# Optimization experiments

Hardware: AMD Instinct MI355X
Metric: run time of the kernel (lower is better)

## Reference

```python
import jax, jax.numpy as jnp
from jax import lax
import numpy as np

B, T, H, K = 32, 512, 2048, 128


def setup_inputs() -> dict:
    key = jax.random.key(0)
    k1, k2, k3, k4, k5, k6, k7 = jax.random.split(key, 7)
    hiddens = jax.random.normal(k1, (B, T, H), dtype=jnp.float32)
    mask = jnp.ones((B, T), dtype=jnp.int32)  # mask[:,0] must be on (torchcrf)
    labels = jax.random.randint(k2, (B, T), 0, K)
    W = jax.random.normal(k3, (H, K), dtype=jnp.float32) * 0.02
    b = jnp.zeros((K,), dtype=jnp.float32)
    # torchcrf inits transitions uniform(-0.1, 0.1)
    start_transitions = jax.random.uniform(k4, (K,), minval=-0.1, maxval=0.1)
    end_transitions = jax.random.uniform(k5, (K,), minval=-0.1, maxval=0.1)
    transitions = jax.random.uniform(k6, (K, K), minval=-0.1, maxval=0.1)
    return {"hiddens": hiddens, "mask": mask, "labels": labels, "W": W, "b": b,
            "start_transitions": start_transitions, "end_transitions": end_transitions,
            "transitions": transitions}


def _crf_log_likelihood(emissions, tags, mask, start_t, end_t, trans):
    # emissions: [B,T,K], tags/mask: [B,T]
    Bn, Tn, Kn = emissions.shape
    maskf = mask.astype(emissions.dtype)
    # ---- numerator: score of the gold path ----
    score = start_t[tags[:, 0]] + emissions[jnp.arange(Bn), 0, tags[:, 0]]
    prev, cur = tags[:, :-1], tags[:, 1:]
    emit_cur = jnp.take_along_axis(emissions[:, 1:], cur[..., None], axis=-1)[..., 0]
    score = score + jnp.sum((trans[prev, cur] + emit_cur) * maskf[:, 1:], axis=1)
    last_idx = mask.sum(axis=1).astype(jnp.int32) - 1
    last_tags = jnp.take_along_axis(tags, last_idx[:, None], axis=1)[:, 0]
    score = score + end_t[last_tags]
    # ---- denominator: log partition via stable logsumexp scan ----
    def step(alpha, inp):
        emit_t, m_t = inp  # [B,K], [B]
        nxt = jax.nn.logsumexp(alpha[:, :, None] + trans[None] + emit_t[:, None, :], axis=1)
        alpha = jnp.where(m_t[:, None] > 0, nxt, alpha)
        return alpha, None
    alpha0 = start_t[None, :] + emissions[:, 0]
    emits = jnp.swapaxes(emissions[:, 1:], 0, 1)  # [T-1,B,K]
    ms = jnp.swapaxes(mask[:, 1:], 0, 1)          # [T-1,B]
    alpha, _ = lax.scan(step, alpha0, (emits, ms))
    logZ = jax.nn.logsumexp(alpha + end_t[None, :], axis=1)
    return score - logZ


def _viterbi_decode(emissions, mask, start_t, end_t, trans):
    Bn, Tn, Kn = emissions.shape
    tag_ids = jnp.arange(Kn, dtype=jnp.int32)
    def step(score, inp):
        emit_t, m_t = inp
        cand = score[:, :, None] + trans[None]          # [B,K,K] prev->cur
        bp = jnp.argmax(cand, axis=1).astype(jnp.int32)  # [B,K]
        best = jnp.max(cand, axis=1) + emit_t
        on = m_t[:, None] > 0
        new_score = jnp.where(on, best, score)
        bp = jnp.where(on, bp, tag_ids[None, :])  # identity for padded steps
        return new_score, bp
    score0 = start_t[None, :] + emissions[:, 0]
    emits = jnp.swapaxes(emissions[:, 1:], 0, 1)
    ms = jnp.swapaxes(mask[:, 1:], 0, 1)
    score, history = lax.scan(step, score0, (emits, ms))  # history: [T-1,B,K]
    last_tag = jnp.argmax(score + end_t[None, :], axis=1).astype(jnp.int32)  # [B]
    def back(tag, bp_t):
        tag = jnp.take_along_axis(bp_t, tag[:, None], axis=1)[:, 0]
        return tag, tag
    _, tags_prev = lax.scan(back, last_tag, history, reverse=True)  # [T-1,B]
    tags = jnp.concatenate([tags_prev, last_tag[None, :]], axis=0)  # [T,B]
    return jnp.swapaxes(tags, 0, 1)  # [B,T]


def reference(hiddens, mask, labels, W, b, start_transitions, end_transitions, transitions):
    logits = jnp.einsum('bth,hk->btk', hiddens, W) + b  # emission projection
    decode = _viterbi_decode(logits, mask, start_transitions, end_transitions, transitions)
    llh = _crf_log_likelihood(logits, labels, mask, start_transitions, end_transitions, transitions)
    loss = -jnp.mean(llh)  # -1 * crf(..., reduction='mean')
    return (decode, loss)
```

## Files before the change

kernel.cpp:

```cpp
#include <hip/hip_runtime.h>
#include <hip/hip_bf16.h>
#include <math.h>

#define BB 32
#define TT 512
#define HH 2048
#define KK 128

__global__ __launch_bounds__(512) void gemm_k(const float* __restrict__ hid,
                                              const float* __restrict__ Wm,
                                              const float* __restrict__ bias,
                                              float* __restrict__ logits,
                                              float* __restrict__ loss_slot) {
    __shared__ union {
        struct { float As[4][16][72]; float Bs[4][16][132]; } s;
        float4 red[16][128];
    } sm;
    const int tid = threadIdx.x, bid = blockIdx.x;
    if (bid == 0 && tid == 0) loss_slot[0] = 0.0f;
    const int g = tid >> 7, lt = tid & 127;
    const int rowBase = bid * 64;
    const int rowg = lt >> 4, colg = lt & 15;
    const int arow = lt >> 1, ahq = lt & 1;

    float acc[8][8];
#pragma unroll
    for (int i = 0; i < 8; i++)
#pragma unroll
        for (int j = 0; j < 8; j++) acc[i][j] = 0.0f;

    const float* hA = hid + (size_t)(rowBase + arow) * HH + g * 512 + ahq * 8;

    for (int it = 0; it < 32; ++it) {
        const int h0 = g * 512 + it * 16;
        float4 a0 = *(const float4*)(hA + it * 16);
        float4 a1 = *(const float4*)(hA + it * 16 + 4);
        float4 bv[4];
#pragma unroll
        for (int r = 0; r < 4; ++r) {
            int idx = r * 128 + lt;
            bv[r] = *(const float4*)(Wm + (size_t)(h0 + (idx >> 5)) * KK + (idx & 31) * 4);
        }
        __syncthreads();
        const int hb = ahq * 8;
        sm.s.As[g][hb + 0][arow] = a0.x;
        sm.s.As[g][hb + 1][arow] = a0.y;
        sm.s.As[g][hb + 2][arow] = a0.z;
        sm.s.As[g][hb + 3][arow] = a0.w;
        sm.s.As[g][hb + 4][arow] = a1.x;
        sm.s.As[g][hb + 5][arow] = a1.y;
        sm.s.As[g][hb + 6][arow] = a1.z;
        sm.s.As[g][hb + 7][arow] = a1.w;
#pragma unroll
        for (int r = 0; r < 4; ++r) {
            int idx = r * 128 + lt;
            *(float4*)&sm.s.Bs[g][idx >> 5][(idx & 31) * 4] = bv[r];
        }
        __syncthreads();
#pragma unroll
        for (int h = 0; h < 16; ++h) {
            float4 aL = *(const float4*)&sm.s.As[g][h][rowg * 8];
            float4 aH = *(const float4*)&sm.s.As[g][h][rowg * 8 + 4];
            float4 b0 = *(const float4*)&sm.s.Bs[g][h][colg * 4];
            float4 b1 = *(const float4*)&sm.s.Bs[g][h][64 + colg * 4];
            float ar[8] = {aL.x, aL.y, aL.z, aL.w, aH.x, aH.y, aH.z, aH.w};
            float br[8] = {b0.x, b0.y, b0.z, b0.w, b1.x, b1.y, b1.z, b1.w};
#pragma unroll
            for (int i = 0; i < 8; i++)
#pragma unroll
                for (int j = 0; j < 8; j++) acc[i][j] = fmaf(ar[i], br[j], acc[i][j]);
        }
    }
    __syncthreads();
    for (int gp = 1; gp <= 3; ++gp) {
        if (g == gp) {
#pragma unroll
            for (int i = 0; i < 8; ++i) {
                sm.red[i * 2][lt] = make_float4(acc[i][0], acc[i][1], acc[i][2], acc[i][3]);
                sm.red[i * 2 + 1][lt] = make_float4(acc[i][4], acc[i][5], acc[i][6], acc[i][7]);
            }
        }
        __syncthreads();
        if (g == 0) {
#pragma unroll
            for (int i = 0; i < 8; ++i) {
                float4 r0 = sm.red[i * 2][lt];
                float4 r1 = sm.red[i * 2 + 1][lt];
                acc[i][0] += r0.x; acc[i][1] += r0.y; acc[i][2] += r0.z; acc[i][3] += r0.w;
                acc[i][4] += r1.x; acc[i][5] += r1.y; acc[i][6] += r1.z; acc[i][7] += r1.w;
            }
        }
        __syncthreads();
    }
    if (g == 0) {
        float4 bb0 = *(const float4*)(bias + colg * 4);
        float4 bb1 = *(const float4*)(bias + 64 + colg * 4);
#pragma unroll
        for (int i = 0; i < 8; ++i) {
            int row = rowBase + rowg * 8 + i;
            *(float4*)(logits + (size_t)row * KK + colg * 4) =
                make_float4(acc[i][0] + bb0.x, acc[i][1] + bb0.y, acc[i][2] + bb0.z, acc[i][3] + bb0.w);
            *(float4*)(logits + (size_t)row * KK + 64 + colg * 4) =
                make_float4(acc[i][4] + bb1.x, acc[i][5] + bb1.y, acc[i][6] + bb1.z, acc[i][7] + bb1.w);
        }
    }
}

struct SMemB {
    float ubuf[2][144];
    float red[4];
    int redi[4];
    float vbuf[128];
};

__global__ __launch_bounds__(256) void scan_k(const float* __restrict__ logits,
                                              const int* __restrict__ mask,
                                              const int* __restrict__ labels,
                                              const float* __restrict__ startT,
                                              const float* __restrict__ endT,
                                              const float* __restrict__ trans,
                                              float* __restrict__ shist,
                                              float* __restrict__ out) {
    __shared__ SMemB sm;
    const int tid = threadIdx.x;
    const int bid = blockIdx.x;
    const float L2E = 1.4426950408889634f;
    const int s = tid & 3;
    const int jb = tid >> 2;
    const int j0 = jb * 2;
    const int padw = j0 + 4 * (j0 >> 5);
    const int lane = tid & 63;

    if (bid < BB) {
        const int b = bid;
        const float* lrow = logits + (size_t)b * TT * KK;
        unsigned long long mb[8];
#pragma unroll
        for (int c = 0; c < 8; ++c) mb[c] = __ballot(mask[b * TT + c * 64 + lane]);
        float V0[32], V1[32];
#pragma unroll
        for (int k = 0; k < 32; k++) {
            V0[k] = exp2f(trans[(s * 32 + k) * KK + j0] * L2E);
            V1[k] = exp2f(trans[(s * 32 + k) * KK + j0 + 1] * L2E);
        }
        float a0_ = (startT[j0] + lrow[j0]) * L2E;
        float a1_ = (startT[j0 + 1] + lrow[j0 + 1]) * L2E;
        float OFF = (startT[0] + lrow[0]) * L2E;
        float S0_ = exp2f(a0_ - OFF);
        float S1_ = exp2f(a1_ - OFF);
        if (s == 0) {
            sm.ubuf[0][padw] = S0_;
            sm.ubuf[0][padw + 1] = S1_;
        }
        __syncthreads();
        int cur = 0;
        float2 em_next = *(const float2*)(lrow + KK + j0);
        for (int t = 1; t < TT; ++t) {
            float2 em = em_next;
            if (t + 1 < TT) em_next = *(const float2*)(lrow + (size_t)(t + 1) * KK + j0);
            int mt = (int)((mb[t >> 6] >> (t & 63)) & 1ull);
            if (mt) {
                const float* ub = &sm.ubuf[cur][s * 36];
                float u00 = sm.ubuf[cur][0];
                float uu[32];
#pragma unroll
                for (int c = 0; c < 8; ++c) {
                    float4 v = *(const float4*)(ub + c * 4);
                    uu[c * 4] = v.x; uu[c * 4 + 1] = v.y; uu[c * 4 + 2] = v.z; uu[c * 4 + 3] = v.w;
                }
                float r00 = __builtin_amdgcn_rcpf(u00);
                float sc0 = exp2f(em.x * L2E) * r00;
                float sc1 = exp2f(em.y * L2E) * r00;
                OFF += log2f(u00);
                float p0e = 0.f, p0o = 0.f, p1e = 0.f, p1o = 0.f;
#pragma unroll
                for (int k = 0; k < 32; k += 2) {
                    p0e = fmaf(uu[k], V0[k], p0e);
                    p1e = fmaf(uu[k], V1[k], p1e);
                    p0o = fmaf(uu[k + 1], V0[k + 1], p0o);
                    p1o = fmaf(uu[k + 1], V1[k + 1], p1o);
                }
                float w0 = p0e + p0o, w1 = p1e + p1o;
                w0 += __shfl_xor(w0, 1, 64);
                w0 += __shfl_xor(w0, 2, 64);
                w1 += __shfl_xor(w1, 1, 64);
                w1 += __shfl_xor(w1, 2, 64);
                S0_ = w0 * sc0;
                S1_ = w1 * sc1;
                if (s == 0) {
                    sm.ubuf[cur ^ 1][padw] = S0_;
                    sm.ubuf[cur ^ 1][padw + 1] = S1_;
                }
                cur ^= 1;
            }
            __syncthreads();
        }
        if (s == 0) {
            sm.vbuf[j0] = log2f(S0_) + endT[j0] * L2E;
            sm.vbuf[j0 + 1] = log2f(S1_) + endT[j0 + 1] * L2E;
        }
        __syncthreads();

        float part = 0.0f;
        for (int tt = tid; tt < TT; tt += 256) {
            if (tt == 0) {
                int l0 = labels[b * TT];
                part += startT[l0] + lrow[l0];
            } else if (mask[b * TT + tt]) {
                int lc = labels[b * TT + tt];
                int lp = labels[b * TT + tt - 1];
                part += trans[lp * KK + lc] + lrow[(size_t)tt * KK + lc];
            }
        }
#pragma unroll
        for (int d = 1; d < 64; d <<= 1) part += __shfl_xor(part, d, 64);
        int wid = tid >> 6;
        if (lane == 0) sm.red[wid] = part;
        __syncthreads();
        if (tid < 64) {
            float v0 = sm.vbuf[tid], v1 = sm.vbuf[tid + 64];
            float mx = fmaxf(v0, v1);
#pragma unroll
            for (int d = 1; d < 64; d <<= 1) mx = fmaxf(mx, __shfl_xor(mx, d, 64));
            float p = exp2f(v0 - mx) + exp2f(v1 - mx);
#pragma unroll
            for (int d = 1; d < 64; d <<= 1) p += __shfl_xor(p, d, 64);
            if (tid == 0) {
                int total = 0;
#pragma unroll
                for (int c = 0; c < 8; ++c) total += __popcll(mb[c]);
                float score = sm.red[0] + sm.red[1] + sm.red[2] + sm.red[3];
                score += endT[labels[b * TT + total - 1]];
                float logZ = (OFF + mx + log2f(p)) * 0.6931471805599453f;
                float llh = score - logZ;
                atomicAdd(out + BB * TT, -llh * (1.0f / 32.0f));
            }
        }
    } else {
        const int b = bid - BB;
        const float* lrow = logits + (size_t)b * TT * KK;
        float* hist = shist + (size_t)b * TT * KK;
        unsigned long long mb[8];
#pragma unroll
        for (int c = 0; c < 8; ++c) mb[c] = __ballot(mask[b * TT + c * 64 + lane]);
        float T0[32], T1[32];
#pragma unroll
        for (int k = 0; k < 32; k++) {
            T0[k] = trans[(s * 32 + k) * KK + j0];
            T1[k] = trans[(s * 32 + k) * KK + j0 + 1];
        }
        float s0_ = startT[j0] + lrow[j0];
        float s1_ = startT[j0 + 1] + lrow[j0 + 1];
        if (s == 0) {
            sm.ubuf[0][padw] = s0_;
            sm.ubuf[0][padw + 1] = s1_;
        } else if (s == 1) {
            *(float2*)(hist + j0) = make_float2(s0_, s1_);
        }
        __syncthreads();
        int cur = 0;
        float2 em_next = *(const float2*)(lrow + KK + j0);
        for (int t = 1; t < TT; ++t) {
            float2 em = em_next;
            if (t + 1 < TT) em_next = *(const float2*)(lrow + (size_t)(t + 1) * KK + j0);
            int mt = (int)((mb[t >> 6] >> (t & 63)) & 1ull);
            if (mt) {
                const float* ub = &sm.ubuf[cur][s * 36];
                float uu[32];
#pragma unroll
                for (int c = 0; c < 8; ++c) {
                    float4 v = *(const float4*)(ub + c * 4);
                    uu[c * 4] = v.x; uu[c * 4 + 1] = v.y; uu[c * 4 + 2] = v.z; uu[c * 4 + 3] = v.w;
                }
                float m0 = -3.0e38f, m1 = -3.0e38f;
#pragma unroll
                for (int k = 0; k < 32; k += 2) {
                    m0 = fmaxf(m0, fmaxf(uu[k] + T0[k], uu[k + 1] + T0[k + 1]));
                    m1 = fmaxf(m1, fmaxf(uu[k] + T1[k], uu[k + 1] + T1[k + 1]));
                }
                m0 = fmaxf(m0, __shfl_xor(m0, 1, 64));
                m0 = fmaxf(m0, __shfl_xor(m0, 2, 64));
                m1 = fmaxf(m1, __shfl_xor(m1, 1, 64));
                m1 = fmaxf(m1, __shfl_xor(m1, 2, 64));
                s0_ = m0 + em.x;
                s1_ = m1 + em.y;
                if (s == 0) {
                    sm.ubuf[cur ^ 1][padw] = s0_;
                    sm.ubuf[cur ^ 1][padw + 1] = s1_;
                } else if (s == 1) {
                    *(float2*)(hist + (size_t)t * KK + j0) = make_float2(s0_, s1_);
                }
                cur ^= 1;
            } else {
                if (s == 1) *(float2*)(hist + (size_t)t * KK + j0) = make_float2(s0_, s1_);
            }
            __syncthreads();
        }
    }
}

__global__ __launch_bounds__(256) void bp_k(const float* __restrict__ shist,
                                            const float* __restrict__ trans,
                                            const int* __restrict__ mask,
                                            unsigned char* __restrict__ bp) {
    const int t = blockIdx.x + 1;
    const int tid = threadIdx.x;
    const int j = tid & 127, bg = tid >> 7;
    __shared__ float sc[BB][KK];
#pragma unroll
    for (int r = 0; r < 4; ++r) {
        int f = tid + r * 256;
        int bb2 = f >> 5, c4 = (f & 31) * 4;
        *(float4*)&sc[bb2][c4] = *(const float4*)&shist[(size_t)bb2 * TT * KK + (size_t)(t - 1) * KK + c4];
    }
    __syncthreads();
    float m[16];
    int idx[16];
#pragma unroll
    for (int c = 0; c < 16; c++) { m[c] = -3.0e38f; idx[c] = 0; }
    for (int i4 = 0; i4 < 32; ++i4) {
        const int ib = i4 * 4;
        float tr0 = trans[(ib + 0) * KK + j];
        float tr1 = trans[(ib + 1) * KK + j];
        float tr2 = trans[(ib + 2) * KK + j];
        float tr3 = trans[(ib + 3) * KK + j];
#pragma unroll
        for (int c = 0; c < 16; c++) {
            float4 s4 = *(const float4*)&sc[bg + 2 * c][ib];
            float c0 = s4.x + tr0, c1 = s4.y + tr1, c2 = s4.z + tr2, c3 = s4.w + tr3;
            if (c0 > m[c]) { m[c] = c0; idx[c] = ib; }
            if (c1 > m[c]) { m[c] = c1; idx[c] = ib + 1; }
            if (c2 > m[c]) { m[c] = c2; idx[c] = ib + 2; }
            if (c3 > m[c]) { m[c] = c3; idx[c] = ib + 3; }
        }
    }
#pragma unroll
    for (int c = 0; c < 16; c++) {
        int bb2 = bg + 2 * c;
        int v = idx[c];
        if (mask[bb2 * TT + t] == 0) v = j;
        bp[(size_t)bb2 * TT * KK + (size_t)t * KK + j] = (unsigned char)v;
    }
}

__global__ __launch_bounds__(512) void bt_k(const float* __restrict__ shist,
                                            const float* __restrict__ endT,
                                            const unsigned char* __restrict__ bp,
                                            float* __restrict__ out) {
    const int b = blockIdx.x;
    const int tid = threadIdx.x;
    const int lane = tid & 63, w = tid >> 6;
    __shared__ float cb[128];
    __shared__ int tagbuf[512];
    __shared__ int handoff;
    if (tid < 128) cb[tid] = shist[(size_t)b * TT * KK + (size_t)(TT - 1) * KK + tid] + endT[tid];
    __syncthreads();
    if (tid == 0) {
        float mm = cb[0];
        int bi = 0;
        for (int i = 1; i < 128; i++)
            if (cb[i] > mm) { mm = cb[i]; bi = i; }
        tagbuf[TT - 1] = bi;
        handoff = bi;
    }
    unsigned int reg[64];
    const unsigned char* bpb = bp + (size_t)b * TT * KK;
#pragma unroll
    for (int r = 0; r < 64; r++) {
        int t_row = w * 64 + 1 + r;
        unsigned int v = 0;
        if (t_row < TT) v = *(const unsigned short*)(bpb + (size_t)t_row * KK + lane * 2);
        reg[r] = v;
    }
    __syncthreads();
    for (int ph = 7; ph >= 0; --ph) {
        if (w == ph) {
            int tag = handoff;
#pragma unroll
            for (int r = 63; r >= 0; --r) {
                int t_row = ph * 64 + 1 + r;
                if (t_row < TT) {
                    unsigned int vv = (unsigned int)__shfl((int)reg[r], tag >> 1, 64);
                    tag = (int)((vv >> ((tag & 1) * 8)) & 0xffu);
                    if (lane == 0) tagbuf[t_row - 1] = tag;
                }
            }
            if (lane == 0) handoff = tag;
        }
        __syncthreads();
    }
    out[b * TT + tid] = (float)tagbuf[tid];
}

extern "C" void kernel_launch(void* const* d_in, const int* in_sizes, int n_in,
                              void* d_out, int out_size, void* d_ws, size_t ws_size,
                              hipStream_t stream) {
    const float* hid = (const float*)d_in[0];
    const int* mask = (const int*)d_in[1];
    const int* labels = (const int*)d_in[2];
    const float* Wm = (const float*)d_in[3];
    const float* bias = (const float*)d_in[4];
    const float* startT = (const float*)d_in[5];
    const float* endT = (const float*)d_in[6];
    const float* trans = (const float*)d_in[7];
    float* out = (float*)d_out;
    char* ws = (char*)d_ws;

    float* logits = (float*)ws;
    float* shist = (float*)(ws + 8388608);
    unsigned char* bp = (unsigned char*)(ws + 16777216);

    gemm_k<<<256, 512, 0, stream>>>(hid, Wm, bias, logits, out + BB * TT);
    scan_k<<<64, 256, 0, stream>>>(logits, mask, labels, startT, endT, trans, shist, out);
    bp_k<<<TT - 1, 256, 0, stream>>>(shist, trans, mask, bp);
    bt_k<<<BB, 512, 0, stream>>>(shist, endT, bp, out);
}
```

Before: 685.8 us.

## Prefetch GEMM tiles and deepen emission prefetch in CRF scans

The GEMM now loads the next k-tile of hiddens and W into registers right after the shared-memory barrier, so global loads overlap the FMA inner loop. Both serial scans keep a 4-deep register queue of emission rows, and the forward scan computes the emission exponentials one step early, taking them off the dependent chain. The inner dot-product and max reductions use four independent accumulators to shorten dependency chains. An unused shared-memory field is dropped. These add register pressure, which could reduce occupancy in the GEMM.

```diff
diff --git a/kernel.cpp b/kernel.cpp
--- a/kernel.cpp
+++ b/kernel.cpp
@@ -31,16 +31,19 @@
 
     const float* hA = hid + (size_t)(rowBase + arow) * HH + g * 512 + ahq * 8;
 
-    for (int it = 0; it < 32; ++it) {
-        const int h0 = g * 512 + it * 16;
-        float4 a0 = *(const float4*)(hA + it * 16);
-        float4 a1 = *(const float4*)(hA + it * 16 + 4);
-        float4 bv[4];
+    float4 a0, a1, bv[4];
+    {
+        const int h0 = g * 512;
+        a0 = *(const float4*)(hA);
+        a1 = *(const float4*)(hA + 4);
 #pragma unroll
         for (int r = 0; r < 4; ++r) {
             int idx = r * 128 + lt;
             bv[r] = *(const float4*)(Wm + (size_t)(h0 + (idx >> 5)) * KK + (idx & 31) * 4);
         }
+    }
+
+    for (int it = 0; it < 32; ++it) {
         __syncthreads();
         const int hb = ahq * 8;
         sm.s.As[g][hb + 0][arow] = a0.x;
@@ -57,6 +60,16 @@
             *(float4*)&sm.s.Bs[g][idx >> 5][(idx & 31) * 4] = bv[r];
         }
         __syncthreads();
+        if (it + 1 < 32) {
+            const int h0 = g * 512 + (it + 1) * 16;
+            a0 = *(const float4*)(hA + (it + 1) * 16);
+            a1 = *(const float4*)(hA + (it + 1) * 16 + 4);
+#pragma unroll
+            for (int r = 0; r < 4; ++r) {
+                int idx = r * 128 + lt;
+                bv[r] = *(const float4*)(Wm + (size_t)(h0 + (idx >> 5)) * KK + (idx & 31) * 4);
+            }
+        }
 #pragma unroll
         for (int h = 0; h < 16; ++h) {
             float4 aL = *(const float4*)&sm.s.As[g][h][rowg * 8];
@@ -109,7 +122,6 @@
 struct SMemB {
     float ubuf[2][144];
     float red[4];
-    int redi[4];
     float vbuf[128];
 };
 
@@ -152,12 +164,17 @@
             sm.ubuf[0][padw] = S0_;
             sm.ubuf[0][padw + 1] = S1_;
         }
+        float2 emq[4];
+#pragma unroll
+        for (int d = 0; d < 4; ++d) emq[d] = *(const float2*)(lrow + (size_t)(1 + d) * KK + j0);
+        float2 scc = make_float2(exp2f(emq[0].x * L2E), exp2f(emq[0].y * L2E));
         __syncthreads();
         int cur = 0;
-        float2 em_next = *(const float2*)(lrow + KK + j0);
         for (int t = 1; t < TT; ++t) {
-            float2 em = em_next;
-            if (t + 1 < TT) em_next = *(const float2*)(lrow + (size_t)(t + 1) * KK + j0);
+            float2 sc = scc;
+            emq[0] = emq[1]; emq[1] = emq[2]; emq[2] = emq[3];
+            if (t + 4 < TT) emq[3] = *(const float2*)(lrow + (size_t)(t + 4) * KK + j0);
+            scc = make_float2(exp2f(emq[0].x * L2E), exp2f(emq[0].y * L2E));
             int mt = (int)((mb[t >> 6] >> (t & 63)) & 1ull);
             if (mt) {
                 const float* ub = &sm.ubuf[cur][s * 36];
@@ -169,24 +186,24 @@
                     uu[c * 4] = v.x; uu[c * 4 + 1] = v.y; uu[c * 4 + 2] = v.z; uu[c * 4 + 3] = v.w;
                 }
                 float r00 = __builtin_amdgcn_rcpf(u00);
-                float sc0 = exp2f(em.x * L2E) * r00;
-                float sc1 = exp2f(em.y * L2E) * r00;
                 OFF += log2f(u00);
-                float p0e = 0.f, p0o = 0.f, p1e = 0.f, p1o = 0.f;
-#pragma unroll
-                for (int k = 0; k < 32; k += 2) {
-                    p0e = fmaf(uu[k], V0[k], p0e);
-                    p1e = fmaf(uu[k], V1[k], p1e);
-                    p0o = fmaf(uu[k + 1], V0[k + 1], p0o);
-                    p1o = fmaf(uu[k + 1], V1[k + 1], p1o);
-                }
-                float w0 = p0e + p0o, w1 = p1e + p1o;
+                float p0[4] = {0.f, 0.f, 0.f, 0.f}, p1[4] = {0.f, 0.f, 0.f, 0.f};
+#pragma unroll
+                for (int k = 0; k < 32; k += 4) {
+#pragma unroll
+                    for (int q = 0; q < 4; ++q) {
+                        p0[q] = fmaf(uu[k + q], V0[k + q], p0[q]);
+                        p1[q] = fmaf(uu[k + q], V1[k + q], p1[q]);
+                    }
+                }
+                float w0 = (p0[0] + p0[1]) + (p0[2] + p0[3]);
+                float w1 = (p1[0] + p1[1]) + (p1[2] + p1[3]);
                 w0 += __shfl_xor(w0, 1, 64);
                 w0 += __shfl_xor(w0, 2, 64);
                 w1 += __shfl_xor(w1, 1, 64);
                 w1 += __shfl_xor(w1, 2, 64);
-                S0_ = w0 * sc0;
-                S1_ = w1 * sc1;
+                S0_ = w0 * (sc.x * r00);
+                S1_ = w1 * (sc.y * r00);
                 if (s == 0) {
                     sm.ubuf[cur ^ 1][padw] = S0_;
                     sm.ubuf[cur ^ 1][padw + 1] = S1_;
@@ -257,12 +274,15 @@
         } else if (s == 1) {
             *(float2*)(hist + j0) = make_float2(s0_, s1_);
         }
+        float2 emq[4];
+#pragma unroll
+        for (int d = 0; d < 4; ++d) emq[d] = *(const float2*)(lrow + (size_t)(1 + d) * KK + j0);
         __syncthreads();
         int cur = 0;
-        float2 em_next = *(const float2*)(lrow + KK + j0);
         for (int t = 1; t < TT; ++t) {
-            float2 em = em_next;
-            if (t + 1 < TT) em_next = *(const float2*)(lrow + (size_t)(t + 1) * KK + j0);
+            float2 em = emq[0];
+            emq[0] = emq[1]; emq[1] = emq[2]; emq[2] = emq[3];
+            if (t + 4 < TT) emq[3] = *(const float2*)(lrow + (size_t)(t + 4) * KK + j0);
             int mt = (int)((mb[t >> 6] >> (t & 63)) & 1ull);
             if (mt) {
                 const float* ub = &sm.ubuf[cur][s * 36];
@@ -272,12 +292,15 @@
                     float4 v = *(const float4*)(ub + c * 4);
                     uu[c * 4] = v.x; uu[c * 4 + 1] = v.y; uu[c * 4 + 2] = v.z; uu[c * 4 + 3] = v.w;
                 }
-                float m0 = -3.0e38f, m1 = -3.0e38f;
-#pragma unroll
-                for (int k = 0; k < 32; k += 2) {
-                    m0 = fmaxf(m0, fmaxf(uu[k] + T0[k], uu[k + 1] + T0[k + 1]));
-                    m1 = fmaxf(m1, fmaxf(uu[k] + T1[k], uu[k + 1] + T1[k + 1]));
-                }
+                float m0a = -3.0e38f, m0b = -3.0e38f, m1a = -3.0e38f, m1b = -3.0e38f;
+#pragma unroll
+                for (int k = 0; k < 32; k += 4) {
+                    m0a = fmaxf(m0a, fmaxf(uu[k] + T0[k], uu[k + 1] + T0[k + 1]));
+                    m0b = fmaxf(m0b, fmaxf(uu[k + 2] + T0[k + 2], uu[k + 3] + T0[k + 3]));
+                    m1a = fmaxf(m1a, fmaxf(uu[k] + T1[k], uu[k + 1] + T1[k + 1]));
+                    m1b = fmaxf(m1b, fmaxf(uu[k + 2] + T1[k + 2], uu[k + 3] + T1[k + 3]));
+                }
+                float m0 = fmaxf(m0a, m0b), m1 = fmaxf(m1a, m1b);
                 m0 = fmaxf(m0, __shfl_xor(m0, 1, 64));
                 m0 = fmaxf(m0, __shfl_xor(m0, 2, 64));
                 m1 = fmaxf(m1, __shfl_xor(m1, 1, 64));
```

Result: faster. 665.4 us (-3.0%).
